# Optimization experiments

Measured on AMD Instinct MI355X. Metric: run time of the kernel, lower is better.

Reference implementation:

```python
import jax, jax.numpy as jnp
import numpy as np

VAR_CXCY = 0.1   # SSD encoding variances
VAR_WH = 0.2
THRESH = 0.5     # match threshold from forward()
EPS = 1e-6


def point_form(p):
    """[P,4] (cx,cy,w,h) -> (x1,y1,x2,y2)."""
    return jnp.concatenate([p[..., :2] - p[..., 2:] / 2,
                            p[..., :2] + p[..., 2:] / 2], axis=-1)


def iou(a, b):
    """a: [N,4] xyxy, b: [P,4] xyxy -> [N,P] jaccard overlap."""
    lt = jnp.maximum(a[:, None, :2], b[None, :, :2])
    rb = jnp.minimum(a[:, None, 2:], b[None, :, 2:])
    wh = jnp.clip(rb - lt, 0.0)
    inter = wh[..., 0] * wh[..., 1]
    area_a = (a[:, 2] - a[:, 0]) * (a[:, 3] - a[:, 1])
    area_b = (b[:, 2] - b[:, 0]) * (b[:, 3] - b[:, 1])
    return inter / (area_a[:, None] + area_b[None, :] - inter + EPS)


def match_one(gt, labels, priors, priors_pt):
    """SSD match for a single image.
    gt: [N,4] xyxy, labels: [N] int, priors: [P,4] cxcywh, priors_pt: [P,4] xyxy.
    Returns loc targets [P,4] and conf targets [P] (0 = background).
    """
    ov = iou(gt, priors_pt)                       # [N,P]
    best_prior_idx = jnp.argmax(ov, axis=1)        # [N] best prior per gt
    best_truth_ov = jnp.max(ov, axis=0)            # [P]
    best_truth_idx = jnp.argmax(ov, axis=0)        # [P] best gt per prior
    n = gt.shape[0]
    # ensure every gt keeps its best prior
    best_truth_ov = best_truth_ov.at[best_prior_idx].set(2.0)
    best_truth_idx = best_truth_idx.at[best_prior_idx].set(jnp.arange(n))
    matches = gt[best_truth_idx]                   # [P,4]
    conf = labels[best_truth_idx] + 1              # shift so 0 = background
    conf = jnp.where(best_truth_ov < THRESH, 0, conf)
    # encode matched boxes relative to priors
    m_cxcy = (matches[:, :2] + matches[:, 2:]) * 0.5
    m_wh = jnp.clip(matches[:, 2:] - matches[:, :2], EPS)
    g_cxcy = (m_cxcy - priors[:, :2]) / (VAR_CXCY * priors[:, 2:])
    g_wh = jnp.log(m_wh / priors[:, 2:]) / VAR_WH
    return jnp.concatenate([g_cxcy, g_wh], axis=1), conf


def setup_inputs() -> dict:
    key = jax.random.key(0)
    k1, k2, k3, k4, k5 = jax.random.split(key, 5)
    B, N, P = 32, 100, 8732
    # ground-truth boxes: valid xyxy corners in [0,1]
    xy1 = jax.random.uniform(k1, (B, N, 2)) * 0.7
    wh = 0.05 + jax.random.uniform(k2, (B, N, 2)) * 0.25
    gt_boxes = jnp.concatenate([xy1, xy1 + wh], axis=-1).astype(jnp.float32)
    gt_labels = jax.random.randint(k3, (B, N), 0, 20)
    # priors: cxcywh
    p_cxcy = jax.random.uniform(k4, (P, 2))
    p_wh = 0.05 + jax.random.uniform(k5, (P, 2)) * 0.45
    priors = jnp.concatenate([p_cxcy, p_wh], axis=-1).astype(jnp.float32)
    return {"gt_boxes": gt_boxes, "gt_labels": gt_labels, "priors": priors}


def reference(gt_boxes, gt_labels, priors):
    priors_pt = point_form(priors)
    loc_t, conf_t = jax.vmap(
        lambda g, l: match_one(g, l, priors, priors_pt))(gt_boxes, gt_labels)
    return loc_t, conf_t
```

## Files before the change

### kernel.cpp

```cpp
#include <hip/hip_runtime.h>

#pragma clang fp contract(off)

#define BB 32
#define NN 100
#define PP 8732
#define CH 16
#define LDW 257
#define NBX 35

template <bool USE_PART>
__global__ __launch_bounds__(256) void k_iou_pass(
    const float* __restrict__ gt,
    const float* __restrict__ priors,
    unsigned long long* __restrict__ red,
    unsigned char* __restrict__ m8)
{
    __shared__ unsigned int s_iou[CH * LDW];
    __shared__ unsigned long long s_part[NN][17];
    __shared__ float s_area[NN];

    const int b = blockIdx.y;
    const int t = threadIdx.x;
    const int p = blockIdx.x * 256 + t;
    const bool valid = p < PP;
    const int pc = valid ? p : (PP - 1);

    const float4* __restrict__ gtb =
        reinterpret_cast<const float4*>(gt) + b * NN;

    if (t < NN) {
        float4 g = gtb[t];
        s_area[t] = (g.z - g.x) * (g.w - g.y);
    }

    const float4 pr = reinterpret_cast<const float4*>(priors)[pc];
    const float px1 = pr.x - pr.z * 0.5f;
    const float py1 = pr.y - pr.w * 0.5f;
    const float px2 = pr.x + pr.z * 0.5f;
    const float py2 = pr.y + pr.w * 0.5f;
    const float area_b = (px2 - px1) * (py2 - py1);

    float best_ov = -1.0f;
    int best_j = 0;

    __syncthreads();

    for (int jc = 0; jc < NN; jc += CH) {
        const int nr = (NN - jc) < CH ? (NN - jc) : CH;

        #pragma unroll
        for (int jj = 0; jj < CH; ++jj) {
            if (jj >= nr) break;
            float4 g = gtb[jc + jj];
            float area_a = s_area[jc + jj];
            float ltx = fmaxf(g.x, px1), lty = fmaxf(g.y, py1);
            float rbx = fminf(g.z, px2), rby = fminf(g.w, py2);
            float w = fmaxf(rbx - ltx, 0.0f), h = fmaxf(rby - lty, 0.0f);
            float inter = w * h;
            float iou = inter / (area_a + area_b - inter + 1e-6f);
            if (iou > best_ov) { best_ov = iou; best_j = jc + jj; }
            s_iou[jj * LDW + t] = __float_as_uint(iou);
        }
        __syncthreads();

        {
            const int r = t & 15;
            const int s = t >> 4;
            if (r < nr) {
                const unsigned int* row = s_iou + r * LDW + s * 16;
                unsigned int bb = row[0];
                int bi = 0;
                #pragma unroll
                for (int i = 1; i < 16; ++i) {
                    unsigned int v = row[i];
                    if (v > bb) { bb = v; bi = i; }
                }
                int pw = blockIdx.x * 256 + s * 16 + bi;
                s_part[jc + r][s] = ((unsigned long long)bb << 32) |
                                    (unsigned int)(~pw);
            }
        }
        __syncthreads();
    }

    if (t < NN) {
        unsigned long long best = s_part[t][0];
        #pragma unroll
        for (int s = 1; s < 16; ++s) {
            unsigned long long k = s_part[t][s];
            if (k > best) best = k;
        }
        if (USE_PART) {
            red[((size_t)b * NBX + blockIdx.x) * NN + t] = best;
        } else {
            atomicMax(&red[b * NN + t], best);
        }
    }
    if (valid) {
        m8[b * PP + p] =
            (unsigned char)(best_j | ((best_ov < 0.5f) ? 0x80 : 0));
    }
}

template <bool USE_PART>
__global__ __launch_bounds__(256) void k_encode(
    const float* __restrict__ gt,
    const int*   __restrict__ labels,
    const float* __restrict__ priors,
    const unsigned long long* __restrict__ red,
    const unsigned char* __restrict__ m8,
    float* __restrict__ loc_out,
    float* __restrict__ conf_out)
{
    __shared__ int s_forced[256];

    const int b = blockIdx.y;
    const int t = threadIdx.x;
    const int p = blockIdx.x * 256 + t;

    s_forced[t] = -1;
    __syncthreads();
    if (t < NN) {
        unsigned long long best;
        if (USE_PART) {
            const unsigned long long* q = red + (size_t)b * NBX * NN + t;
            best = q[0];
            #pragma unroll 5
            for (int bx = 1; bx < NBX; ++bx) {
                unsigned long long k = q[(size_t)bx * NN];
                if (k > best) best = k;
            }
        } else {
            best = red[b * NN + t];
        }
        int kp = (int)~(unsigned int)(best & 0xFFFFFFFFull);
        int lp = kp - blockIdx.x * 256;
        if ((unsigned)lp < 256u) atomicMax(&s_forced[lp], t);
    }
    __syncthreads();

    if (p >= PP) return;
    const int forced_j = s_forced[t];

    const unsigned char m = m8[b * PP + p];
    const int j    = (forced_j >= 0) ? forced_j : (m & 0x7f);
    const int lab  = labels[b * NN + j];
    const int conf = (forced_j < 0 && (m & 0x80)) ? 0 : (lab + 1);

    const float4 pr = reinterpret_cast<const float4*>(priors)[p];
    const float4 g  = reinterpret_cast<const float4*>(gt)[b * NN + j];
    const float mcx = (g.x + g.z) * 0.5f;
    const float mcy = (g.y + g.w) * 0.5f;
    const float mw  = fmaxf(g.z - g.x, 1e-6f);
    const float mh  = fmaxf(g.w - g.y, 1e-6f);
    const float gcx = (mcx - pr.x) / (0.1f * pr.z);
    const float gcy = (mcy - pr.y) / (0.1f * pr.w);
    const float gw  = logf(mw / pr.z) / 0.2f;
    const float gh  = logf(mh / pr.w) / 0.2f;

    reinterpret_cast<float4*>(loc_out)[b * PP + p] =
        make_float4(gcx, gcy, gw, gh);
    conf_out[b * PP + p] = (float)conf;
}

extern "C" void kernel_launch(void* const* d_in, const int* in_sizes, int n_in,
                              void* d_out, int out_size, void* d_ws, size_t ws_size,
                              hipStream_t stream) {
    const float* gt     = (const float*)d_in[0];
    const int*   labels = (const int*)  d_in[1];
    const float* priors = (const float*)d_in[2];

    float* loc  = (float*)d_out;
    float* conf = (float*)d_out + (size_t)BB * PP * 4;

    const size_t part_bytes = (size_t)BB * NBX * NN * 8;
    const size_t m8_bytes   = (size_t)BB * PP;
    dim3 grid(NBX, BB);

    if (ws_size >= part_bytes + m8_bytes) {
        unsigned long long* part = (unsigned long long*)d_ws;
        unsigned char* m8 = (unsigned char*)d_ws + part_bytes;
        k_iou_pass<true><<<grid, 256, 0, stream>>>(gt, priors, part, m8);
        k_encode<true><<<grid, 256, 0, stream>>>(gt, labels, priors, part,
                                                 m8, loc, conf);
    } else {
        unsigned long long* gkey = (unsigned long long*)d_ws;
        unsigned char* m8 = (unsigned char*)d_ws + (size_t)BB * NN * 8;
        hipMemsetAsync(gkey, 0, (size_t)BB * NN * 8, stream);
        k_iou_pass<false><<<grid, 256, 0, stream>>>(gt, priors, gkey, m8);
        k_encode<false><<<grid, 256, 0, stream>>>(gt, labels, priors, gkey,
                                                  m8, loc, conf);
    }
}
```

Before: 96.60 us.

## Fuse encoding into IoU pass and patch only forced-match priors afterward

```diff
diff --git a/kernel.cpp b/kernel.cpp
--- a/kernel.cpp
+++ b/kernel.cpp
@@ -9,12 +9,25 @@
 #define LDW 257
 #define NBX 35
 
+__device__ __forceinline__ float4 encode_box(float4 g, float4 pr) {
+    const float mcx = (g.x + g.z) * 0.5f;
+    const float mcy = (g.y + g.w) * 0.5f;
+    const float mw  = fmaxf(g.z - g.x, 1e-6f);
+    const float mh  = fmaxf(g.w - g.y, 1e-6f);
+    return make_float4((mcx - pr.x) / (0.1f * pr.z),
+                       (mcy - pr.y) / (0.1f * pr.w),
+                       logf(mw / pr.z) / 0.2f,
+                       logf(mh / pr.w) / 0.2f);
+}
+
 template <bool USE_PART>
 __global__ __launch_bounds__(256) void k_iou_pass(
     const float* __restrict__ gt,
+    const int*   __restrict__ labels,
     const float* __restrict__ priors,
     unsigned long long* __restrict__ red,
-    unsigned char* __restrict__ m8)
+    float* __restrict__ loc_out,
+    float* __restrict__ conf_out)
 {
     __shared__ unsigned int s_iou[CH * LDW];
     __shared__ unsigned long long s_part[NN][17];
@@ -97,30 +110,31 @@
             atomicMax(&red[b * NN + t], best);
         }
     }
+
     if (valid) {
-        m8[b * PP + p] =
-            (unsigned char)(best_j | ((best_ov < 0.5f) ? 0x80 : 0));
+        const int lab  = labels[b * NN + best_j];
+        const int conf = (best_ov < 0.5f) ? 0 : (lab + 1);
+        const float4 g = gtb[best_j];
+        reinterpret_cast<float4*>(loc_out)[b * PP + p] = encode_box(g, pr);
+        conf_out[b * PP + p] = (float)conf;
     }
 }
 
 template <bool USE_PART>
-__global__ __launch_bounds__(256) void k_encode(
+__global__ __launch_bounds__(128) void k_patch(
     const float* __restrict__ gt,
     const int*   __restrict__ labels,
     const float* __restrict__ priors,
     const unsigned long long* __restrict__ red,
-    const unsigned char* __restrict__ m8,
     float* __restrict__ loc_out,
     float* __restrict__ conf_out)
 {
-    __shared__ int s_forced[256];
+    __shared__ int s_kp[NN];
 
-    const int b = blockIdx.y;
+    const int b = blockIdx.x;
     const int t = threadIdx.x;
-    const int p = blockIdx.x * 256 + t;
 
-    s_forced[t] = -1;
-    __syncthreads();
+    int kp = -1;
     if (t < NN) {
         unsigned long long best;
         if (USE_PART) {
@@ -134,34 +148,22 @@
         } else {
             best = red[b * NN + t];
         }
-        int kp = (int)~(unsigned int)(best & 0xFFFFFFFFull);
-        int lp = kp - blockIdx.x * 256;
-        if ((unsigned)lp < 256u) atomicMax(&s_forced[lp], t);
+        kp = (int)~(unsigned int)(best & 0xFFFFFFFFull);
+        s_kp[t] = kp;
     }
     __syncthreads();
 
-    if (p >= PP) return;
-    const int forced_j = s_forced[t];
-
-    const unsigned char m = m8[b * PP + p];
-    const int j    = (forced_j >= 0) ? forced_j : (m & 0x7f);
-    const int lab  = labels[b * NN + j];
-    const int conf = (forced_j < 0 && (m & 0x80)) ? 0 : (lab + 1);
-
-    const float4 pr = reinterpret_cast<const float4*>(priors)[p];
-    const float4 g  = reinterpret_cast<const float4*>(gt)[b * NN + j];
-    const float mcx = (g.x + g.z) * 0.5f;
-    const float mcy = (g.y + g.w) * 0.5f;
-    const float mw  = fmaxf(g.z - g.x, 1e-6f);
-    const float mh  = fmaxf(g.w - g.y, 1e-6f);
-    const float gcx = (mcx - pr.x) / (0.1f * pr.z);
-    const float gcy = (mcy - pr.y) / (0.1f * pr.w);
-    const float gw  = logf(mw / pr.z) / 0.2f;
-    const float gh  = logf(mh / pr.w) / 0.2f;
-
-    reinterpret_cast<float4*>(loc_out)[b * PP + p] =
-        make_float4(gcx, gcy, gw, gh);
-    conf_out[b * PP + p] = (float)conf;
+    if (t < NN) {
+        bool win = true;
+        for (int u = t + 1; u < NN; ++u)
+            if (s_kp[u] == kp) { win = false; break; }
+        if (win) {
+            const float4 g  = reinterpret_cast<const float4*>(gt)[b * NN + t];
+            const float4 pr = reinterpret_cast<const float4*>(priors)[kp];
+            reinterpret_cast<float4*>(loc_out)[b * PP + kp] = encode_box(g, pr);
+            conf_out[b * PP + kp] = (float)(labels[b * NN + t] + 1);
+        }
+    }
 }
 
 extern "C" void kernel_launch(void* const* d_in, const int* in_sizes, int n_in,
@@ -175,21 +177,20 @@
     float* conf = (float*)d_out + (size_t)BB * PP * 4;
 
     const size_t part_bytes = (size_t)BB * NBX * NN * 8;
-    const size_t m8_bytes   = (size_t)BB * PP;
     dim3 grid(NBX, BB);
 
-    if (ws_size >= part_bytes + m8_bytes) {
+    if (ws_size >= part_bytes) {
         unsigned long long* part = (unsigned long long*)d_ws;
-        unsigned char* m8 = (unsigned char*)d_ws + part_bytes;
-        k_iou_pass<true><<<grid, 256, 0, stream>>>(gt, priors, part, m8);
-        k_encode<true><<<grid, 256, 0, stream>>>(gt, labels, priors, part,
-                                                 m8, loc, conf);
+        k_iou_pass<true><<<grid, 256, 0, stream>>>(gt, labels, priors, part,
+                                                   loc, conf);
+        k_patch<true><<<BB, 128, 0, stream>>>(gt, labels, priors, part,
+                                              loc, conf);
     } else {
         unsigned long long* gkey = (unsigned long long*)d_ws;
-        unsigned char* m8 = (unsigned char*)d_ws + (size_t)BB * NN * 8;
         hipMemsetAsync(gkey, 0, (size_t)BB * NN * 8, stream);
-        k_iou_pass<false><<<grid, 256, 0, stream>>>(gt, priors, gkey, m8);
-        k_encode<false><<<grid, 256, 0, stream>>>(gt, labels, priors, gkey,
-                                                  m8, loc, conf);
+        k_iou_pass<false><<<grid, 256, 0, stream>>>(gt, labels, priors, gkey,
+                                                    loc, conf);
+        k_patch<false><<<BB, 128, 0, stream>>>(gt, labels, priors, gkey,
+                                               loc, conf);
     }
 }
```

New measurement: 104.0 us. +7.7%, slower.

## Split IoU pass across two GT halves per block with 128 priors each

Applied to the files above, without the earlier changes.

```diff
diff --git a/kernel.cpp b/kernel.cpp
--- a/kernel.cpp
+++ b/kernel.cpp
@@ -5,8 +5,10 @@
 #define BB 32
 #define NN 100
 #define PP 8732
-#define CH 16
-#define LDW 257
+#define HJ 50
+#define CHH 8
+#define LDW 129
+#define NBK 69
 #define NBX 35
 
 template <bool USE_PART>
@@ -16,23 +18,19 @@
     unsigned long long* __restrict__ red,
     unsigned char* __restrict__ m8)
 {
-    __shared__ unsigned int s_iou[CH * LDW];
+    __shared__ unsigned int s_iou[2 * CHH * LDW];
     __shared__ unsigned long long s_part[NN][17];
-    __shared__ float s_area[NN];
-
-    const int b = blockIdx.y;
-    const int t = threadIdx.x;
-    const int p = blockIdx.x * 256 + t;
+
+    const int b    = blockIdx.y;
+    const int t    = threadIdx.x;
+    const int tc   = t & 127;
+    const int half = t >> 7;
+    const int p    = blockIdx.x * 128 + tc;
     const bool valid = p < PP;
     const int pc = valid ? p : (PP - 1);
 
     const float4* __restrict__ gtb =
         reinterpret_cast<const float4*>(gt) + b * NN;
-
-    if (t < NN) {
-        float4 g = gtb[t];
-        s_area[t] = (g.z - g.x) * (g.w - g.y);
-    }
 
     const float4 pr = reinterpret_cast<const float4*>(priors)[pc];
     const float px1 = pr.x - pr.z * 0.5f;
@@ -41,47 +39,61 @@
     const float py2 = pr.y + pr.w * 0.5f;
     const float area_b = (px2 - px1) * (py2 - py1);
 
-    float best_ov = -1.0f;
-    int best_j = 0;
-
-    __syncthreads();
-
-    for (int jc = 0; jc < NN; jc += CH) {
-        const int nr = (NN - jc) < CH ? (NN - jc) : CH;
+    float bo = -1.0f;
+    int bj = half * HJ;
+
+    for (int jc = 0; jc < HJ; jc += CHH) {
+        const int nr = (HJ - jc) < CHH ? (HJ - jc) : CHH;
 
         #pragma unroll
-        for (int jj = 0; jj < CH; ++jj) {
+        for (int jj = 0; jj < CHH; ++jj) {
             if (jj >= nr) break;
-            float4 g = gtb[jc + jj];
-            float area_a = s_area[jc + jj];
+            const int j = half * HJ + jc + jj;
+            float4 g = gtb[j];
+            float area_a = (g.z - g.x) * (g.w - g.y);
             float ltx = fmaxf(g.x, px1), lty = fmaxf(g.y, py1);
             float rbx = fminf(g.z, px2), rby = fminf(g.w, py2);
             float w = fmaxf(rbx - ltx, 0.0f), h = fmaxf(rby - lty, 0.0f);
             float inter = w * h;
             float iou = inter / (area_a + area_b - inter + 1e-6f);
-            if (iou > best_ov) { best_ov = iou; best_j = jc + jj; }
-            s_iou[jj * LDW + t] = __float_as_uint(iou);
+            if (iou > bo) { bo = iou; bj = j; }
+            s_iou[(half * CHH + jj) * LDW + tc] = __float_as_uint(iou);
         }
         __syncthreads();
 
         {
-            const int r = t & 15;
-            const int s = t >> 4;
-            if (r < nr) {
-                const unsigned int* row = s_iou + r * LDW + s * 16;
+            const int r  = t & 15;
+            const int s  = t >> 4;
+            const int rr = r & 7;
+            if (rr < nr) {
+                const unsigned int* row = s_iou + r * LDW + s * 8;
                 unsigned int bb = row[0];
                 int bi = 0;
                 #pragma unroll
-                for (int i = 1; i < 16; ++i) {
+                for (int i = 1; i < 8; ++i) {
                     unsigned int v = row[i];
                     if (v > bb) { bb = v; bi = i; }
                 }
-                int pw = blockIdx.x * 256 + s * 16 + bi;
-                s_part[jc + r][s] = ((unsigned long long)bb << 32) |
-                                    (unsigned int)(~pw);
+                int pw = blockIdx.x * 128 + s * 8 + bi;
+                int jrow = (r >> 3) * HJ + jc + rr;
+                s_part[jrow][s] = ((unsigned long long)bb << 32) |
+                                  (unsigned int)(~pw);
             }
         }
         __syncthreads();
+    }
+
+    unsigned long long* s_mrg = (unsigned long long*)s_iou;
+    unsigned long long ck = ((unsigned long long)__float_as_uint(bo) << 32) |
+                            (unsigned int)(~bj);
+    if (half) s_mrg[tc] = ck;
+    __syncthreads();
+    if (!half && valid) {
+        unsigned long long o = s_mrg[tc];
+        if (o > ck) ck = o;
+        float fo = __uint_as_float((unsigned int)(ck >> 32));
+        int fj = (int)~(unsigned int)ck;
+        m8[b * PP + p] = (unsigned char)(fj | ((fo < 0.5f) ? 0x80 : 0));
     }
 
     if (t < NN) {
@@ -92,14 +104,10 @@
             if (k > best) best = k;
         }
         if (USE_PART) {
-            red[((size_t)b * NBX + blockIdx.x) * NN + t] = best;
+            red[((size_t)b * NBK + blockIdx.x) * NN + t] = best;
         } else {
             atomicMax(&red[b * NN + t], best);
         }
-    }
-    if (valid) {
-        m8[b * PP + p] =
-            (unsigned char)(best_j | ((best_ov < 0.5f) ? 0x80 : 0));
     }
 }
 
@@ -124,10 +132,10 @@
     if (t < NN) {
         unsigned long long best;
         if (USE_PART) {
-            const unsigned long long* q = red + (size_t)b * NBX * NN + t;
+            const unsigned long long* q = red + (size_t)b * NBK * NN + t;
             best = q[0];
-            #pragma unroll 5
-            for (int bx = 1; bx < NBX; ++bx) {
+            #pragma unroll 4
+            for (int bx = 1; bx < NBK; ++bx) {
                 unsigned long long k = q[(size_t)bx * NN];
                 if (k > best) best = k;
             }
@@ -174,22 +182,23 @@
     float* loc  = (float*)d_out;
     float* conf = (float*)d_out + (size_t)BB * PP * 4;
 
-    const size_t part_bytes = (size_t)BB * NBX * NN * 8;
+    const size_t part_bytes = (size_t)BB * NBK * NN * 8;
     const size_t m8_bytes   = (size_t)BB * PP;
-    dim3 grid(NBX, BB);
+    dim3 giou(NBK, BB);
+    dim3 genc(NBX, BB);
 
     if (ws_size >= part_bytes + m8_bytes) {
         unsigned long long* part = (unsigned long long*)d_ws;
         unsigned char* m8 = (unsigned char*)d_ws + part_bytes;
-        k_iou_pass<true><<<grid, 256, 0, stream>>>(gt, priors, part, m8);
-        k_encode<true><<<grid, 256, 0, stream>>>(gt, labels, priors, part,
+        k_iou_pass<true><<<giou, 256, 0, stream>>>(gt, priors, part, m8);
+        k_encode<true><<<genc, 256, 0, stream>>>(gt, labels, priors, part,
                                                  m8, loc, conf);
     } else {
         unsigned long long* gkey = (unsigned long long*)d_ws;
         unsigned char* m8 = (unsigned char*)d_ws + (size_t)BB * NN * 8;
         hipMemsetAsync(gkey, 0, (size_t)BB * NN * 8, stream);
-        k_iou_pass<false><<<grid, 256, 0, stream>>>(gt, priors, gkey, m8);
-        k_encode<false><<<grid, 256, 0, stream>>>(gt, labels, priors, gkey,
+        k_iou_pass<false><<<giou, 256, 0, stream>>>(gt, priors, gkey, m8);
+        k_encode<false><<<genc, 256, 0, stream>>>(gt, labels, priors, gkey,
                                                   m8, loc, conf);
     }
 }
```

After: 97.36 us. Within noise of the previous version (+0.8%).
